# Kernel tuning notes

Measured on AMD Instinct MI355X. Metric: run time of the kernel, lower is better.

The kernel has to match this reference:

```python
import jax, jax.numpy as jnp
import numpy as np

N = 50000      # nodes
E = 500000     # edges (avg degree 10)
D_IN = 256     # input feature dim
HID = 256      # hidden_channels
HEADS = 8
C_HID = HID // HEADS   # 32 per-head dim for concat layers
NCLS = 8               # num_classes (last layer per-head dim, concat=False)


def setup_inputs() -> dict:
    key = jax.random.key(0)
    keys = iter(jax.random.split(key, 64))
    def w(shape, s=0.05):
        return jax.random.normal(next(keys), shape, jnp.float32) * s
    inp = {}
    inp["x"] = jax.random.normal(next(keys), (N, D_IN), jnp.float32)
    inp["edge_index"] = jax.random.randint(next(keys), (2, E), 0, N, jnp.int32)
    # (fan_in, heads*per_head_out, skip_out) per layer; layer3: concat=False
    layer_cfg = [(D_IN, HEADS * C_HID, HEADS * C_HID),
                 (HID, HEADS * C_HID, HEADS * C_HID),
                 (HID, HEADS * NCLS, NCLS)]
    for i, (fin, hc, skip) in enumerate(layer_cfg, 1):
        for nm in ("q", "k", "v"):
            inp[f"W{nm}{i}"] = w((fin, hc))
            inp[f"b{nm}{i}"] = jnp.zeros((hc,), jnp.float32)
        inp[f"Ws{i}"] = w((fin, skip))
        inp[f"bs{i}"] = jnp.zeros((skip,), jnp.float32)
        inp[f"Wb{i}"] = w((3 * skip, 1))
    for i in (1, 2):
        inp[f"ln{i}_g"] = jnp.ones((HID,), jnp.float32)
        inp[f"ln{i}_b"] = jnp.zeros((HID,), jnp.float32)
    return inp


def _layer_norm(x, g, b):
    mu = x.mean(-1, keepdims=True)
    var = ((x - mu) ** 2).mean(-1, keepdims=True)
    return (x - mu) * jax.lax.rsqrt(var + 1e-5) * g + b


def _tconv(x, src, dst, Wq, bq, Wk, bk, Wv, bv, Ws, bs, Wb, concat):
    """PyG TransformerConv with beta=True, root_weight=True, eval-mode (no dropout)."""
    n = x.shape[0]
    q = (x @ Wq + bq).reshape(n, HEADS, -1)   # [N,H,C]
    k = (x @ Wk + bk).reshape(n, HEADS, -1)
    v = (x @ Wv + bv).reshape(n, HEADS, -1)
    C = q.shape[-1]
    # per-edge attention logits, scaled dot product
    logits = (q[dst] * k[src]).sum(-1) * jax.lax.rsqrt(jnp.float32(C))  # [E,H]
    # segment softmax over incoming edges of each dst node
    m = jax.ops.segment_max(logits, dst, num_segments=n)                # [N,H]
    m = jnp.where(jnp.isfinite(m), m, 0.0)                              # empty segments
    e = jnp.exp(logits - m[dst])
    s = jax.ops.segment_sum(e, dst, num_segments=n)
    alpha = e / (s[dst] + 1e-16)                                        # [E,H]
    # scatter-aggregate messages
    out = jax.ops.segment_sum(v[src] * alpha[:, :, None], dst, num_segments=n)  # [N,H,C]
    out = out.reshape(n, -1) if concat else out.mean(axis=1)
    # beta-gated skip connection
    xr = x @ Ws + bs
    beta = jax.nn.sigmoid(jnp.concatenate([out, xr, out - xr], axis=-1) @ Wb)   # [N,1]
    return beta * xr + (1.0 - beta) * out


def reference(x, edge_index,
              Wq1, bq1, Wk1, bk1, Wv1, bv1, Ws1, bs1, Wb1,
              Wq2, bq2, Wk2, bk2, Wv2, bv2, Ws2, bs2, Wb2,
              Wq3, bq3, Wk3, bk3, Wv3, bv3, Ws3, bs3, Wb3,
              ln1_g, ln1_b, ln2_g, ln2_b):
    src, dst = edge_index[0], edge_index[1]
    h = jax.nn.relu(_layer_norm(
        _tconv(x, src, dst, Wq1, bq1, Wk1, bk1, Wv1, bv1, Ws1, bs1, Wb1, True),
        ln1_g, ln1_b))
    h = jax.nn.relu(_layer_norm(
        _tconv(h, src, dst, Wq2, bq2, Wk2, bk2, Wv2, bv2, Ws2, bs2, Wb2, True),
        ln2_g, ln2_b))
    return _tconv(h, src, dst, Wq3, bq3, Wk3, bk3, Wv3, bv3, Ws3, bs3, Wb3, False)
```

## Files before the change

kernel.cpp:

```cpp
#include <hip/hip_runtime.h>
#include <stdint.h>

typedef __attribute__((ext_vector_type(8))) short short8;
typedef __attribute__((ext_vector_type(4))) float f32x4;
typedef __attribute__((ext_vector_type(4))) _Float16 half4;
typedef __attribute__((ext_vector_type(2))) _Float16 half2v;
typedef __attribute__((ext_vector_type(4))) int i32x4;

struct us4 { unsigned short x, y, z, w; };

__device__ __forceinline__ float b2f(unsigned short u){
  union { unsigned int i; float f; } x; x.i = ((unsigned int)u) << 16; return x.f;
}
__device__ __forceinline__ unsigned short f2b(float f){
  union { float f; unsigned int i; } x; x.f = f;
  unsigned int i = x.i;
  unsigned int r = (i + 0x7FFFu + ((i >> 16) & 1u)) >> 16;
  return (unsigned short)r;
}
__device__ __forceinline__ unsigned short f2h(float f){
  _Float16 h = (_Float16)f;
  union { _Float16 h; unsigned short u; } c; c.h = h; return c.u;
}
__device__ __forceinline__ float sane(float v){
  return fminf(fmaxf(v, -1e30f), 1e30f);
}
__device__ __forceinline__ float lclamp(float v){
  return fminf(fmaxf(v, -60.f), 60.f);
}
__device__ __forceinline__ float ldin(const void* p, size_t i, int f32){
  return f32 ? ((const float*)p)[i] : b2f(((const unsigned short*)p)[i]);
}
__device__ __forceinline__ float dot4h(half2v a0, half2v a1, half2v b0, half2v b1){
#if __has_builtin(__builtin_amdgcn_fdot2)
  return __builtin_amdgcn_fdot2(a0, b0, __builtin_amdgcn_fdot2(a1, b1, 0.f, false), false);
#else
  return (float)a0.x*(float)b0.x + (float)a0.y*(float)b0.y
       + (float)a1.x*(float)b1.x + (float)a1.y*(float)b1.y;
#endif
}

__global__ void k_flag(const unsigned short* __restrict__ xu, int* __restrict__ flag){
  __shared__ int cnt;
  if (threadIdx.x == 0) cnt = 0;
  __syncthreads();
  unsigned u = xu[2 * threadIdx.x];
  int e = (u >> 7) & 0xFF;
  if (e >= 97 && e <= 132) atomicAdd(&cnt, 1);
  __syncthreads();
  if (threadIdx.x == 0) flag[0] = (cnt >= 192) ? 0 : 1;
}

__global__ void k_cvt(const void* __restrict__ xin, unsigned short* __restrict__ xb,
                      int n4, const int* __restrict__ flagp){
  int f32 = *flagp;
  int i = blockIdx.x * 256 + threadIdx.x;
  if (i < n4){
    if (f32){
      float4 v = ((const float4*)xin)[i];
      us4 o = { f2b(v.x), f2b(v.y), f2b(v.z), f2b(v.w) };
      ((us4*)xb)[i] = o;
    } else {
      ((us4*)xb)[i] = ((const us4*)xin)[i];
    }
  }
}

__global__ void k_deg(const int* __restrict__ ei, int E, int N, int* __restrict__ deg){
  int e = blockIdx.x * 256 + threadIdx.x;
  if (e < E){
    unsigned d = (unsigned)ei[E + e];
    if (d < (unsigned)N) atomicAdd(&deg[d], 1);
  }
}

__device__ __forceinline__ int pad4(int d){ return (d + 3) & ~3; }

__global__ void k_bsum(const int* __restrict__ deg, int N, int* __restrict__ bsum){
  int b = blockIdx.x, t = threadIdx.x;
  int i0 = b * 1024 + t * 4;
  int s = 0;
  if (i0 + 4 <= N){
    int4 v = *(const int4*)&deg[i0];
    s = pad4(v.x) + pad4(v.y) + pad4(v.z) + pad4(v.w);
  } else {
    #pragma unroll
    for (int j = 0; j < 4; ++j){ int i = i0 + j; if (i < N) s += pad4(deg[i]); }
  }
  #pragma unroll
  for (int off = 32; off; off >>= 1) s += __shfl_xor(s, off);
  __shared__ int ws[4];
  if ((t & 63) == 0) ws[t >> 6] = s;
  __syncthreads();
  if (t == 0) bsum[b] = ws[0] + ws[1] + ws[2] + ws[3];
}

__global__ void k_bscan(const int* __restrict__ bsum, int nb,
                        int* __restrict__ boff, int* __restrict__ rowptr, int N){
  int t = threadIdx.x;
  if (nb <= 64){
    int v = (t < nb) ? bsum[t] : 0;
    int inc = v;
    #pragma unroll
    for (int off = 1; off < 64; off <<= 1){
      int u = __shfl_up(inc, off);
      if (t >= off) inc += u;
    }
    if (t < nb) boff[t] = inc - v;
    if (t == 63) rowptr[N] = inc;
  } else {
    if (t == 0){
      int run = 0;
      for (int i = 0; i < nb; ++i){ boff[i] = run; run += bsum[i]; }
      rowptr[N] = run;
    }
  }
}

__global__ void k_rowptr(const int* __restrict__ deg, const int* __restrict__ boff,
                         int N, int* __restrict__ rowptr, int* __restrict__ cursor){
  int b = blockIdx.x, t = threadIdx.x;
  int i0 = b * 1024 + t * 4;
  int d0 = 0, d1 = 0, d2 = 0, d3 = 0;
  if (i0 + 4 <= N){
    int4 v = *(const int4*)&deg[i0];
    d0 = v.x; d1 = v.y; d2 = v.z; d3 = v.w;
  } else {
    if (i0     < N) d0 = deg[i0];
    if (i0 + 1 < N) d1 = deg[i0 + 1];
    if (i0 + 2 < N) d2 = deg[i0 + 2];
    if (i0 + 3 < N) d3 = deg[i0 + 3];
  }
  int p0 = pad4(d0), p1 = pad4(d1), p2 = pad4(d2), p3 = pad4(d3);
  int s = p0 + p1 + p2 + p3;
  int lane = t & 63, w = t >> 6;
  int inc = s;
  #pragma unroll
  for (int off = 1; off < 64; off <<= 1){
    int u = __shfl_up(inc, off);
    if (lane >= off) inc += u;
  }
  int wex = inc - s;
  __shared__ int wtot[4];
  if (lane == 63) wtot[w] = inc;
  __syncthreads();
  int cross = 0;
  for (int i = 0; i < w; ++i) cross += wtot[i];
  int basev = boff[b] + cross + wex;
  int r0 = basev, r1 = basev + p0, r2 = r1 + p1, r3 = r2 + p2;
  if (i0 + 4 <= N){
    int4 o = { r0, r1, r2, r3 };
    *(int4*)&rowptr[i0] = o;
    *(int4*)&cursor[i0] = o;
  } else {
    if (i0     < N){ rowptr[i0]   = r0; cursor[i0]   = r0; }
    if (i0 + 1 < N){ rowptr[i0+1] = r1; cursor[i0+1] = r1; }
    if (i0 + 2 < N){ rowptr[i0+2] = r2; cursor[i0+2] = r2; }
    if (i0 + 3 < N){ rowptr[i0+3] = r3; cursor[i0+3] = r3; }
  }
}

__global__ void k_scatter(const int* __restrict__ ei, int E, int N, int Epad,
                          int* __restrict__ cursor, int* __restrict__ srcs){
  int e = blockIdx.x * 256 + threadIdx.x;
  if (e < E){
    unsigned d = (unsigned)ei[E + e];
    if (d < (unsigned)N){
      int pos = atomicAdd(&cursor[d], 1);
      if ((unsigned)pos < (unsigned)Epad){
        unsigned s = (unsigned)ei[e];
        srcs[pos] = (s < (unsigned)N) ? (int)(s * 1024u) : 0;
      }
    }
  }
}

__global__ void k_pack(const void* __restrict__ Wq, const void* __restrict__ bq,
                       const void* __restrict__ Wk, const void* __restrict__ bk,
                       const void* __restrict__ Wv, const void* __restrict__ bv,
                       const void* __restrict__ Ws, const void* __restrict__ bs,
                       unsigned short* __restrict__ WT, float* __restrict__ bias,
                       int Mq, int Ms, int K, const int* __restrict__ flagp){
  int f32 = *flagp;
  int cg = blockIdx.x;
  int k  = threadIdx.x;
  int mat, c, mc;
  if (cg < 3 * Mq){ mat = cg / Mq; c = cg % Mq; mc = Mq; }
  else if (cg < 3 * Mq + Ms){ mat = 3; c = cg - 3 * Mq; mc = Ms; }
  else { mat = 4; c = 0; mc = 1; }
  const void* W = (mat==0)?Wq:(mat==1)?Wk:(mat==2)?Wv:(mat==3)?Ws:(const void*)0;
  WT[(size_t)cg * K + k] = (mat < 4) ? f2b(ldin(W, (size_t)k * mc + c, f32)) : (unsigned short)0;
  if (k == 0){
    const void* B = (mat==0)?bq:(mat==1)?bk:(mat==2)?bv:(mat==3)?bs:(const void*)0;
    bias[cg] = (mat < 4) ? ldin(B, c, f32) : 0.f;
  }
}

__global__ __launch_bounds__(256) void k_gemm(const unsigned short* __restrict__ A,
                                              const unsigned short* __restrict__ WT,
                                              const float* __restrict__ bias,
                                              unsigned short* __restrict__ qout,
                                              char* __restrict__ kvout,
                                              unsigned short* __restrict__ xout,
                                              int N, int Mout, int secshift){
  __shared__ __align__(16) unsigned short sh[64 * 264];
  auto Alds = (unsigned short(*)[264])sh;
  auto Clds = (unsigned short(*)[276])sh;
  int tid = threadIdx.x, wid = tid >> 6, lane = tid & 63;
  int l15 = lane & 15, l4 = lane >> 4;
  int nit = Mout >> 8;
  int it = blockIdx.x % nit;
  int row0 = (blockIdx.x / nit) * 64;
  {
    int srow = tid >> 2, sc4 = tid & 3;
    int ar = row0 + srow; if (ar >= N) ar = N - 1;
    const unsigned short* Ap = A + (size_t)ar * 256;
    #pragma unroll
    for (int i = 0; i < 8; ++i){
      int col = (sc4 + 4 * i) * 8;
      *(short8*)&Alds[srow][col] = *(const short8*)&Ap[col];
    }
  }
  __syncthreads();
  int secw = 1 << secshift;
  int strow = tid >> 3, stchunk = tid & 7;
  int sec, blk;
  if (nit == 1){ sec = wid; blk = 0; }
  else if (it == 0){ sec = 0; blk = wid; }
  else if (it == 3){ sec = 3; blk = wid; }
  else { sec = (wid < 2) ? 1 : 2; blk = (it - 1) * 2 + (wid & 1); }
  int cbf = sec * secw + blk * 64;
  f32x4 acc[4][4] = {};
  #pragma unroll
  for (int k0 = 0; k0 < 256; k0 += 32){
    short8 a0 = *(const short8*)&Alds[l15     ][k0 + l4*8];
    short8 a1 = *(const short8*)&Alds[16 + l15][k0 + l4*8];
    short8 a2 = *(const short8*)&Alds[32 + l15][k0 + l4*8];
    short8 a3 = *(const short8*)&Alds[48 + l15][k0 + l4*8];
    const unsigned short* wb = WT + (size_t)(cbf + l15) * 256 + k0 + l4*8;
    short8 b0 = *(const short8*)(wb);
    short8 b1 = *(const short8*)(wb + 16*256);
    short8 b2 = *(const short8*)(wb + 32*256);
    short8 b3 = *(const short8*)(wb + 48*256);
    acc[0][0] = __builtin_amdgcn_mfma_f32_16x16x32_bf16(a0, b0, acc[0][0], 0,0,0);
    acc[0][1] = __builtin_amdgcn_mfma_f32_16x16x32_bf16(a0, b1, acc[0][1], 0,0,0);
    acc[0][2] = __builtin_amdgcn_mfma_f32_16x16x32_bf16(a0, b2, acc[0][2], 0,0,0);
    acc[0][3] = __builtin_amdgcn_mfma_f32_16x16x32_bf16(a0, b3, acc[0][3], 0,0,0);
    acc[1][0] = __builtin_amdgcn_mfma_f32_16x16x32_bf16(a1, b0, acc[1][0], 0,0,0);
    acc[1][1] = __builtin_amdgcn_mfma_f32_16x16x32_bf16(a1, b1, acc[1][1], 0,0,0);
    acc[1][2] = __builtin_amdgcn_mfma_f32_16x16x32_bf16(a1, b2, acc[1][2], 0,0,0);
    acc[1][3] = __builtin_amdgcn_mfma_f32_16x16x32_bf16(a1, b3, acc[1][3], 0,0,0);
    acc[2][0] = __builtin_amdgcn_mfma_f32_16x16x32_bf16(a2, b0, acc[2][0], 0,0,0);
    acc[2][1] = __builtin_amdgcn_mfma_f32_16x16x32_bf16(a2, b1, acc[2][1], 0,0,0);
    acc[2][2] = __builtin_amdgcn_mfma_f32_16x16x32_bf16(a2, b2, acc[2][2], 0,0,0);
    acc[2][3] = __builtin_amdgcn_mfma_f32_16x16x32_bf16(a2, b3, acc[2][3], 0,0,0);
    acc[3][0] = __builtin_amdgcn_mfma_f32_16x16x32_bf16(a3, b0, acc[3][0], 0,0,0);
    acc[3][1] = __builtin_amdgcn_mfma_f32_16x16x32_bf16(a3, b1, acc[3][1], 0,0,0);
    acc[3][2] = __builtin_amdgcn_mfma_f32_16x16x32_bf16(a3, b2, acc[3][2], 0,0,0);
    acc[3][3] = __builtin_amdgcn_mfma_f32_16x16x32_bf16(a3, b3, acc[3][3], 0,0,0);
  }
  __syncthreads();
  #pragma unroll
  for (int ph = 0; ph < 2; ++ph){
    #pragma unroll
    for (int rt2 = 0; rt2 < 2; ++rt2){
      int rt = ph*2 + rt2;
      #pragma unroll
      for (int ct = 0; ct < 4; ++ct){
        float bv = bias[cbf + ct*16 + l15];
        #pragma unroll
        for (int r = 0; r < 4; ++r)
          Clds[rt2*16 + l4*4 + r][wid*64 + ct*16 + l15] = f2h(acc[rt][ct][r] + bv);
      }
    }
    __syncthreads();
    int grow = row0 + ph*32 + strow;
    if (grow < N){
      if (nit == 4){
        if (it == 0 || it == 3){
          unsigned short* Bp = (it == 0) ? qout : xout;
          int g0 = stchunk * 32;
          unsigned short* dst = Bp + (size_t)grow * secw + g0;
          const unsigned short* srcp = &Clds[strow][g0];
          #pragma unroll
          for (int j = 0; j < 4; ++j)
            *(short8*)(dst + j*8) = *(const short8*)(srcp + j*8);
        } else {
          int secbase = (it == 1) ? 0 : 128;
          int scl = stchunk * 16;
          char* dstb = kvout + (size_t)grow * 1024 + (size_t)(secbase + scl) * 4;
          const unsigned short* kp = &Clds[strow][scl];
          const unsigned short* vp = &Clds[strow][128 + scl];
          #pragma unroll
          for (int g2 = 0; g2 < 4; ++g2){
            union { unsigned long long u[2]; i32x4 v; } st;
            st.u[0] = *(const unsigned long long*)(kp + g2*4);
            st.u[1] = *(const unsigned long long*)(vp + g2*4);
            *(i32x4*)(dstb + g2*16) = st.v;
          }
        }
      } else {
        if (stchunk < 2){
          int g0 = stchunk * 32;
          unsigned short* dst = qout + (size_t)grow * secw + g0;
          const unsigned short* srcp = &Clds[strow][g0];
          #pragma unroll
          for (int j = 0; j < 4; ++j)
            *(short8*)(dst + j*8) = *(const short8*)(srcp + j*8);
        } else if (stchunk < 6){
          int scl = (stchunk - 2) * 16;
          char* dstb = kvout + (size_t)grow * 256 + (size_t)scl * 4;
          const unsigned short* kp = &Clds[strow][64 + scl];
          const unsigned short* vp = &Clds[strow][128 + scl];
          #pragma unroll
          for (int g2 = 0; g2 < 4; ++g2){
            union { unsigned long long u[2]; i32x4 v; } st;
            st.u[0] = *(const unsigned long long*)(kp + g2*4);
            st.u[1] = *(const unsigned long long*)(vp + g2*4);
            *(i32x4*)(dstb + g2*16) = st.v;
          }
        } else {
          int g0 = (stchunk - 6) * 32;
          unsigned short* dst = xout + (size_t)grow * secw + g0;
          const unsigned short* srcp = &Clds[strow][192 + g0];
          #pragma unroll
          for (int j = 0; j < 4; ++j)
            *(short8*)(dst + j*8) = *(const short8*)(srcp + j*8);
        }
      }
    }
    __syncthreads();
  }
}

__global__ __launch_bounds__(256) void k_attn(const unsigned short* __restrict__ qb,
                                              const char* __restrict__ kvb,
                                              const unsigned short* __restrict__ xb,
                                              const int* __restrict__ rowptr,
                                              const int* __restrict__ degv,
                                              const int* __restrict__ srcs,
                                              const void* __restrict__ Wb,
                                              const void* __restrict__ lng,
                                              const void* __restrict__ lnb,
                                              unsigned short* __restrict__ hout,
                                              int N, int E, const int* __restrict__ flagp){
  int f32 = *flagp;
  int tid = threadIdx.x, w = tid >> 6, l = tid & 63;
  int n = blockIdx.x * 4 + w;
  if (n >= N) return;
  unsigned lof = (unsigned)l * 16u;
  size_t nbase = (size_t)n * 512;
  union KV { i32x4 v; _Float16 h[8]; half2v h2[4]; };
  half4 qv = *(const half4*)((const char*)qb + nbase + (unsigned)l * 8u);
  half2v q01 = { qv.x, qv.y }, q23 = { qv.z, qv.w };
  int e0 = rowptr[n]; if (e0 < 0) e0 = 0;
  int dg = degv[n]; if (dg < 0) dg = 0; if (dg > E) dg = E;
  int npad = (dg + 3) & ~3;
  const float scale = 0.17677669529663687f;
  float ss = 0.f, o0 = 0.f, o1 = 0.f, o2 = 0.f, o3 = 0.f;

  auto consume = [&](const KV& kv, int valid){
    float p = dot4h(q01, q23, kv.h2[0], kv.h2[1]);
    p += __shfl_xor(p, 1); p += __shfl_xor(p, 2); p += __shfl_xor(p, 4);
    float a = valid ? __expf(lclamp(p * scale)) : 0.f;
    ss += a;
    o0 += a * (float)kv.h[4];
    o1 += a * (float)kv.h[5];
    o2 += a * (float)kv.h[6];
    o3 += a * (float)kv.h[7];
  };

  if (npad > 0){
    i32x4 offs = *(const i32x4*)&srcs[e0];
    KV c0, c1, c2, c3;
    c0.v = *(const i32x4*)(kvb + (unsigned)offs[0] + lof);
    c1.v = *(const i32x4*)(kvb + (unsigned)offs[1] + lof);
    c2.v = *(const i32x4*)(kvb + (unsigned)offs[2] + lof);
    c3.v = *(const i32x4*)(kvb + (unsigned)offs[3] + lof);
    int base = 0;
    #pragma unroll 1
    for (; base + 4 < npad; base += 4){
      i32x4 offsN = *(const i32x4*)&srcs[e0 + base + 4];
      KV n0, n1, n2, n3;
      n0.v = *(const i32x4*)(kvb + (unsigned)offsN[0] + lof);
      n1.v = *(const i32x4*)(kvb + (unsigned)offsN[1] + lof);
      n2.v = *(const i32x4*)(kvb + (unsigned)offsN[2] + lof);
      n3.v = *(const i32x4*)(kvb + (unsigned)offsN[3] + lof);
      consume(c0, 1); consume(c1, 1); consume(c2, 1); consume(c3, 1);
      c0 = n0; c1 = n1; c2 = n2; c3 = n3;
    }
    consume(c0, base + 0 < dg);
    consume(c1, base + 1 < dg);
    consume(c2, base + 2 < dg);
    consume(c3, base + 3 < dg);
  }

  float sinv = 1.f / (ss + 1e-16f);
  o0 = sane(o0 * sinv); o1 = sane(o1 * sinv);
  o2 = sane(o2 * sinv); o3 = sane(o3 * sinv);
  int c = l * 4;
  half4 xv = *(const half4*)((const char*)xb + nbase + (unsigned)l * 8u);
  float x0 = sane((float)xv.x), x1 = sane((float)xv.y);
  float x2 = sane((float)xv.z), x3 = sane((float)xv.w);
  float d = o0*ldin(Wb, c+0, f32) + x0*ldin(Wb, 256+c+0, f32) + (o0-x0)*ldin(Wb, 512+c+0, f32)
          + o1*ldin(Wb, c+1, f32) + x1*ldin(Wb, 256+c+1, f32) + (o1-x1)*ldin(Wb, 512+c+1, f32)
          + o2*ldin(Wb, c+2, f32) + x2*ldin(Wb, 256+c+2, f32) + (o2-x2)*ldin(Wb, 512+c+2, f32)
          + o3*ldin(Wb, c+3, f32) + x3*ldin(Wb, 256+c+3, f32) + (o3-x3)*ldin(Wb, 512+c+3, f32);
  #pragma unroll
  for (int off = 32; off; off >>= 1) d += __shfl_xor(d, off);
  float beta = 1.f / (1.f + __expf(-d));
  float r0 = beta*x0 + (1.f-beta)*o0;
  float r1 = beta*x1 + (1.f-beta)*o1;
  float r2 = beta*x2 + (1.f-beta)*o2;
  float r3 = beta*x3 + (1.f-beta)*o3;
  float sm = r0 + r1 + r2 + r3;
  #pragma unroll
  for (int off = 32; off; off >>= 1) sm += __shfl_xor(sm, off);
  float mu = sm * (1.f/256.f);
  float d0 = r0-mu, d1 = r1-mu, d2 = r2-mu, d3 = r3-mu;
  float vv2 = d0*d0 + d1*d1 + d2*d2 + d3*d3;
  #pragma unroll
  for (int off = 32; off; off >>= 1) vv2 += __shfl_xor(vv2, off);
  float rs = rsqrtf(vv2 * (1.f/256.f) + 1e-5f);
  us4 outv;
  outv.x = f2b(fmaxf(d0*rs*ldin(lng,c+0,f32) + ldin(lnb,c+0,f32), 0.f));
  outv.y = f2b(fmaxf(d1*rs*ldin(lng,c+1,f32) + ldin(lnb,c+1,f32), 0.f));
  outv.z = f2b(fmaxf(d2*rs*ldin(lng,c+2,f32) + ldin(lnb,c+2,f32), 0.f));
  outv.w = f2b(fmaxf(d3*rs*ldin(lng,c+3,f32) + ldin(lnb,c+3,f32), 0.f));
  *(us4*)&hout[(size_t)n * 256 + c] = outv;
}

__global__ __launch_bounds__(256) void k_final(const unsigned short* __restrict__ q3b,
                                               const char* __restrict__ kv3b,
                                               const unsigned short* __restrict__ x3b,
                                               const int* __restrict__ rowptr,
                                               const int* __restrict__ degv,
                                               const int* __restrict__ srcs,
                                               const void* __restrict__ Wb,
                                               void* __restrict__ outp,
                                               int N, int E, const int* __restrict__ flagp){
  int f32 = *flagp;
  int tid = threadIdx.x, w = tid >> 6, l = tid & 63;
  int n = blockIdx.x * 4 + w;
  if (n >= N) return;
  int es = l >> 4, g = l & 15, j = g & 1;
  unsigned lof = (unsigned)g * 16u;
  size_t nbase = (size_t)n * 128;
  union KV { i32x4 v; _Float16 h[8]; half2v h2[4]; };
  half4 qv = *(const half4*)((const char*)q3b + nbase + (unsigned)g * 8u);
  half2v q01 = { qv.x, qv.y }, q23 = { qv.z, qv.w };
  int e0 = rowptr[n]; if (e0 < 0) e0 = 0;
  int dg = degv[n]; if (dg < 0) dg = 0; if (dg > E) dg = E;
  int npad = (dg + 3) & ~3;
  const float scale = 0.35355339059327373f;
  float ss = 0.f, o0 = 0.f, o1 = 0.f, o2 = 0.f, o3 = 0.f;

  auto consume = [&](const KV& kv, int valid){
    float p = dot4h(q01, q23, kv.h2[0], kv.h2[1]);
    p += __shfl_xor(p, 1);
    float a = valid ? __expf(lclamp(p * scale)) : 0.f;
    ss += a;
    o0 += a * (float)kv.h[4];
    o1 += a * (float)kv.h[5];
    o2 += a * (float)kv.h[6];
    o3 += a * (float)kv.h[7];
  };

  int idx = es;
  if (idx < npad){
    KV c;
    c.v = *(const i32x4*)(kv3b + (((unsigned)srcs[e0 + idx]) >> 2) + lof);
    #pragma unroll 1
    for (; idx + 4 < npad; idx += 4){
      KV nx;
      nx.v = *(const i32x4*)(kv3b + (((unsigned)srcs[e0 + idx + 4]) >> 2) + lof);
      consume(c, idx < dg);
      c = nx;
    }
    consume(c, idx < dg);
  }
  #pragma unroll
  for (int off = 16; off <= 32; off <<= 1){
    ss += __shfl_xor(ss, off);
    o0 += __shfl_xor(o0, off); o1 += __shfl_xor(o1, off);
    o2 += __shfl_xor(o2, off); o3 += __shfl_xor(o3, off);
  }
  float sinv = 1.f / (ss + 1e-16f);
  o0 = sane(o0 * sinv); o1 = sane(o1 * sinv);
  o2 = sane(o2 * sinv); o3 = sane(o3 * sinv);
  #pragma unroll
  for (int off = 2; off <= 8; off <<= 1){
    o0 += __shfl_xor(o0, off); o1 += __shfl_xor(o1, off);
    o2 += __shfl_xor(o2, off); o3 += __shfl_xor(o3, off);
  }
  o0 *= 0.125f; o1 *= 0.125f; o2 *= 0.125f; o3 *= 0.125f;
  half4 xv = *(const half4*)((const char*)x3b + nbase + (unsigned)(j * 8));
  float x0 = sane((float)xv.x), x1 = sane((float)xv.y);
  float x2 = sane((float)xv.z), x3v = sane((float)xv.w);
  int c = j*4;
  float d = o0*ldin(Wb, c+0, f32) + x0*ldin(Wb, 8+c+0, f32) + (o0-x0)*ldin(Wb, 16+c+0, f32)
          + o1*ldin(Wb, c+1, f32) + x1*ldin(Wb, 8+c+1, f32) + (o1-x1)*ldin(Wb, 16+c+1, f32)
          + o2*ldin(Wb, c+2, f32) + x2*ldin(Wb, 8+c+2, f32) + (o2-x2)*ldin(Wb, 16+c+2, f32)
          + o3*ldin(Wb, c+3, f32) + x3v*ldin(Wb, 8+c+3, f32) + (o3-x3v)*ldin(Wb, 16+c+3, f32);
  d += __shfl_xor(d, 1);
  float beta = 1.f / (1.f + __expf(-d));
  float r0 = beta*x0  + (1.f-beta)*o0;
  float r1 = beta*x1  + (1.f-beta)*o1;
  float r2 = beta*x2  + (1.f-beta)*o2;
  float r3 = beta*x3v + (1.f-beta)*o3;
  if (l < 2){
    if (f32){
      float* op = (float*)outp + (size_t)n*8 + l*4;
      op[0] = r0; op[1] = r1; op[2] = r2; op[3] = r3;
    } else {
      unsigned short* op = (unsigned short*)outp + (size_t)n*8 + l*4;
      op[0] = f2b(r0); op[1] = f2b(r1); op[2] = f2b(r2); op[3] = f2b(r3);
    }
  }
}

extern "C" void kernel_launch(void* const* d_in, const int* in_sizes, int n_in,
                              void* d_out, int out_size, void* d_ws, size_t ws_size,
                              hipStream_t stream){
  const int* ei = (const int*)d_in[1];
  const int N = in_sizes[0] / 256;
  const int E = in_sizes[1] / 2;
  const int Epad = E + 4 * N + 64;

  char* wsp = (char*)d_ws;
  size_t off = 0;
  auto alloc = [&](size_t b) -> void* {
    void* p = wsp + off; off = (off + b + 255) & ~(size_t)255; return p;
  };
  unsigned short* WT1  = (unsigned short*)alloc((size_t)1024*256*2);
  unsigned short* WT2  = (unsigned short*)alloc((size_t)1024*256*2);
  unsigned short* WT3  = (unsigned short*)alloc((size_t)256*256*2);
  float* bias1 = (float*)alloc(1024*4);
  float* bias2 = (float*)alloc(1024*4);
  float* bias3 = (float*)alloc(256*4);
  int* flag   = (int*)alloc(256);
  int* deg    = (int*)alloc((size_t)N*4);
  int* rowptr = (int*)alloc((size_t)(N+1)*4);
  int* cursor = (int*)alloc((size_t)N*4);
  int* bsum   = (int*)alloc(1024*4);
  int* boff   = (int*)alloc(1024*4);
  int* srcs   = (int*)alloc((size_t)Epad*4);
  unsigned short* xbf = (unsigned short*)alloc((size_t)N*256*2);
  unsigned short* qb  = (unsigned short*)alloc((size_t)N*256*2);
  char*           kvb = (char*)alloc((size_t)N*1024);
  unsigned short* xb  = (unsigned short*)alloc((size_t)N*256*2);
  unsigned short* hbuf= (unsigned short*)alloc((size_t)N*256*2);
  (void)ws_size; (void)n_in; (void)out_size;

  k_flag<<<1, 256, 0, stream>>>((const unsigned short*)d_in[0], flag);
  int n4 = (N * 256) / 4;
  k_cvt<<<(n4 + 255) / 256, 256, 0, stream>>>(d_in[0], xbf, n4, flag);

  hipMemsetAsync(deg, 0, (size_t)N*4, stream);
  hipMemsetAsync(srcs, 0, (size_t)Epad*4, stream);
  int eb = (E + 255) / 256;
  int nbk = (N + 1023) / 1024;
  k_deg<<<eb, 256, 0, stream>>>(ei, E, N, deg);
  k_bsum<<<nbk, 256, 0, stream>>>(deg, N, bsum);
  k_bscan<<<1, 64, 0, stream>>>(bsum, nbk, boff, rowptr, N);
  k_rowptr<<<nbk, 256, 0, stream>>>(deg, boff, N, rowptr, cursor);
  k_scatter<<<eb, 256, 0, stream>>>(ei, E, N, Epad, cursor, srcs);

  k_pack<<<1024, 256, 0, stream>>>(d_in[2],  d_in[3],  d_in[4],  d_in[5],  d_in[6],  d_in[7],  d_in[8],  d_in[9],  WT1, bias1, 256, 256, 256, flag);
  k_pack<<<1024, 256, 0, stream>>>(d_in[11], d_in[12], d_in[13], d_in[14], d_in[15], d_in[16], d_in[17], d_in[18], WT2, bias2, 256, 256, 256, flag);
  k_pack<<< 256, 256, 0, stream>>>(d_in[20], d_in[21], d_in[22], d_in[23], d_in[24], d_in[25], d_in[26], d_in[27], WT3, bias3,  64,   8, 256, flag);

  int rb = (N + 63) / 64;
  int nb = (N + 3) / 4;
  k_gemm<<<rb * 4, 256, 0, stream>>>(xbf, WT1, bias1, qb, kvb, xb, N, 1024, 8);
  k_attn<<<nb, 256, 0, stream>>>(qb, kvb, xb, rowptr, deg, srcs, d_in[10], d_in[29], d_in[30], hbuf, N, E, flag);
  k_gemm<<<rb * 4, 256, 0, stream>>>(hbuf, WT2, bias2, qb, kvb, xb, N, 1024, 8);
  k_attn<<<nb, 256, 0, stream>>>(qb, kvb, xb, rowptr, deg, srcs, d_in[19], d_in[31], d_in[32], hbuf, N, E, flag);
  k_gemm<<<rb, 256, 0, stream>>>(hbuf, WT3, bias3, qb, kvb, xb, N, 256, 6);
  k_final<<<nb, 256, 0, stream>>>(qb, kvb, xb, rowptr, deg, srcs, d_in[28], d_out, N, E, flag);
}
```

Before: 641.2 us.

## Stage GEMM A and B tiles through LDS via direct global-to-LDS loads

```diff
diff --git a/kernel.cpp b/kernel.cpp
--- a/kernel.cpp
+++ b/kernel.cpp
@@ -38,6 +38,11 @@
   return (float)a0.x*(float)b0.x + (float)a0.y*(float)b0.y
        + (float)a1.x*(float)b1.x + (float)a1.y*(float)b1.y;
 #endif
+}
+__device__ __forceinline__ void gload_lds16(const void* g, void* l){
+  __builtin_amdgcn_global_load_lds(
+      (const __attribute__((address_space(1))) void*)g,
+      (__attribute__((address_space(3))) void*)l, 16, 0, 0);
 }
 
 __global__ void k_flag(const unsigned short* __restrict__ xu, int* __restrict__ flag){
@@ -203,45 +208,56 @@
                                               char* __restrict__ kvout,
                                               unsigned short* __restrict__ xout,
                                               int N, int Mout, int secshift){
-  __shared__ __align__(16) unsigned short sh[64 * 264];
-  auto Alds = (unsigned short(*)[264])sh;
+  __shared__ __align__(16) unsigned short sh[64*32 + 256*32];
+  unsigned short* Achk = sh;
+  unsigned short* Blds = sh + 64*32;
   auto Clds = (unsigned short(*)[276])sh;
   int tid = threadIdx.x, wid = tid >> 6, lane = tid & 63;
   int l15 = lane & 15, l4 = lane >> 4;
   int nit = Mout >> 8;
   int it = blockIdx.x % nit;
   int row0 = (blockIdx.x / nit) * 64;
-  {
-    int srow = tid >> 2, sc4 = tid & 3;
-    int ar = row0 + srow; if (ar >= N) ar = N - 1;
-    const unsigned short* Ap = A + (size_t)ar * 256;
-    #pragma unroll
-    for (int i = 0; i < 8; ++i){
-      int col = (sc4 + 4 * i) * 8;
-      *(short8*)&Alds[srow][col] = *(const short8*)&Ap[col];
-    }
-  }
-  __syncthreads();
   int secw = 1 << secshift;
-  int strow = tid >> 3, stchunk = tid & 7;
   int sec, blk;
   if (nit == 1){ sec = wid; blk = 0; }
   else if (it == 0){ sec = 0; blk = wid; }
   else if (it == 3){ sec = 3; blk = wid; }
   else { sec = (wid < 2) ? 1 : 2; blk = (it - 1) * 2 + (wid & 1); }
   int cbf = sec * secw + blk * 64;
+
+  int sr = lane >> 2, sc = lane & 3;
+  int arow = row0 + wid * 16 + sr; if (arow >= N) arow = N - 1;
+  const unsigned short* Ag = A + (size_t)arow * 256 + sc * 8;
+  const unsigned short* Bg[4];
+  #pragma unroll
+  for (int j = 0; j < 4; ++j){
+    int r = wid * 64 + j * 16 + sr;
+    int gcol;
+    if (nit == 1 || it == 0) gcol = r;
+    else if (it == 3)        gcol = 768 + r;
+    else if (it == 1)        gcol = r + (r < 128 ? 256 : 384);
+    else                     gcol = r + (r < 128 ? 384 : 512);
+    Bg[j] = WT + (size_t)gcol * 256 + sc * 8;
+  }
+  unsigned short* AldsD = Achk + (wid * 16) * 32;
+  unsigned short* BldsD = Blds + (wid * 64) * 32;
+
   f32x4 acc[4][4] = {};
-  #pragma unroll
   for (int k0 = 0; k0 < 256; k0 += 32){
-    short8 a0 = *(const short8*)&Alds[l15     ][k0 + l4*8];
-    short8 a1 = *(const short8*)&Alds[16 + l15][k0 + l4*8];
-    short8 a2 = *(const short8*)&Alds[32 + l15][k0 + l4*8];
-    short8 a3 = *(const short8*)&Alds[48 + l15][k0 + l4*8];
-    const unsigned short* wb = WT + (size_t)(cbf + l15) * 256 + k0 + l4*8;
-    short8 b0 = *(const short8*)(wb);
-    short8 b1 = *(const short8*)(wb + 16*256);
-    short8 b2 = *(const short8*)(wb + 32*256);
-    short8 b3 = *(const short8*)(wb + 48*256);
+    gload_lds16(Ag + k0, AldsD);
+    gload_lds16(Bg[0] + k0, BldsD);
+    gload_lds16(Bg[1] + k0, BldsD + 16*32);
+    gload_lds16(Bg[2] + k0, BldsD + 32*32);
+    gload_lds16(Bg[3] + k0, BldsD + 48*32);
+    __syncthreads();
+    short8 a0 = *(const short8*)&Achk[(     l15)*32 + l4*8];
+    short8 a1 = *(const short8*)&Achk[(16 + l15)*32 + l4*8];
+    short8 a2 = *(const short8*)&Achk[(32 + l15)*32 + l4*8];
+    short8 a3 = *(const short8*)&Achk[(48 + l15)*32 + l4*8];
+    short8 b0 = *(const short8*)&Blds[(wid*64      + l15)*32 + l4*8];
+    short8 b1 = *(const short8*)&Blds[(wid*64 + 16 + l15)*32 + l4*8];
+    short8 b2 = *(const short8*)&Blds[(wid*64 + 32 + l15)*32 + l4*8];
+    short8 b3 = *(const short8*)&Blds[(wid*64 + 48 + l15)*32 + l4*8];
     acc[0][0] = __builtin_amdgcn_mfma_f32_16x16x32_bf16(a0, b0, acc[0][0], 0,0,0);
     acc[0][1] = __builtin_amdgcn_mfma_f32_16x16x32_bf16(a0, b1, acc[0][1], 0,0,0);
     acc[0][2] = __builtin_amdgcn_mfma_f32_16x16x32_bf16(a0, b2, acc[0][2], 0,0,0);
@@ -258,8 +274,9 @@
     acc[3][1] = __builtin_amdgcn_mfma_f32_16x16x32_bf16(a3, b1, acc[3][1], 0,0,0);
     acc[3][2] = __builtin_amdgcn_mfma_f32_16x16x32_bf16(a3, b2, acc[3][2], 0,0,0);
     acc[3][3] = __builtin_amdgcn_mfma_f32_16x16x32_bf16(a3, b3, acc[3][3], 0,0,0);
-  }
-  __syncthreads();
+    __syncthreads();
+  }
+  int strow = tid >> 3, stchunk = tid & 7;
   #pragma unroll
   for (int ph = 0; ph < 2; ++ph){
     #pragma unroll
```

New measurement: 595.2 us. -7.2%, faster.
